# Performance work log

Measured on AMD Instinct MI355X. Metric: run time of the kernel, lower is better.

Reference implementation:

```python
import jax, jax.numpy as jnp
import numpy as np

B, CLN, QL, IH, IW = 64, 32, 32, 16, 16
CDF, SL = 256, 128
IDF = CLN * IH * IW  # 8192


def setup_inputs() -> dict:
    key = jax.random.key(0)
    k1, k2, k3 = jax.random.split(key, 3)
    inp = jax.random.normal(k1, (B, CLN, QL, IH, IW), dtype=jnp.float32)
    context = jax.random.normal(k2, (B, CDF, SL), dtype=jnp.float32)
    # Conv2d(cdf, idf, 1, bias=False) weight, squeezed to [idf, cdf]
    W = jax.random.normal(k3, (IDF, CDF), dtype=jnp.float32) * (1.0 / np.sqrt(CDF))
    return {"input": inp, "context": context, "W": W}


def reference(input, context, W):
    b, cln, queryL, ih, iw = input.shape
    idf = cln * ih * iw
    sourceL = context.shape[2]
    # target: b x queryL x (cln*ih*iw)
    targetT = jnp.transpose(input, (0, 2, 1, 3, 4)).reshape(b, queryL, idf)
    # 1x1 conv projection of context: b x idf x sourceL
    sourceT = jnp.einsum('oc,bcs->bos', W, context)
    # attention scores and softmax over sourceL (nn.Softmax on 2D -> dim=1)
    attn = jnp.einsum('bqd,bds->bqs', targetT, sourceT)  # b x queryL x sourceL
    attn = jax.nn.softmax(attn, axis=-1)
    attnT = jnp.transpose(attn, (0, 2, 1))  # b x sourceL x queryL
    # weighted context: b x idf x queryL
    wc = jnp.einsum('bds,bsq->bdq', sourceT, attnT)
    # faithful to torch .view: raw row-major reinterpretation of [b, idf, queryL]
    wc = wc.reshape(b, queryL, cln, ih, iw)
    wc = jnp.transpose(wc, (0, 2, 1, 3, 4))  # b x cln x queryL x ih x iw
    return (wc, attnT)
```

## Files before the change

kernel.cpp:

```cpp
#include <hip/hip_runtime.h>
#include <math.h>


#define ZK 16

typedef _Float16 f16x8 __attribute__((ext_vector_type(8)));
typedef __fp16 h16x2 __attribute__((ext_vector_type(2)));
typedef float f32x4 __attribute__((ext_vector_type(4)));

#define GLDS16(gp, lp)                                                          \
    __builtin_amdgcn_global_load_lds(                                           \
        (const __attribute__((address_space(1))) void*)(gp),                    \
        (__attribute__((address_space(3))) void*)(lp), 16, 0, 0)

__global__ __launch_bounds__(256) void k0a_prep(const float* __restrict__ Wm,
                                                _Float16* __restrict__ Wth,
                                                _Float16* __restrict__ Wtl) {
    const int kb = blockIdx.x;
    const int t = threadIdx.x;
    __shared__ float tile[32][260];
    {
        const int r = t >> 3;
        const int c0 = (t & 7) * 32;
        const float* src = Wm + (long)(kb * 32 + r) * 256 + c0;
#pragma unroll
        for (int i = 0; i < 8; ++i) {
            float4 v = *(const float4*)(src + i * 4);
            tile[r][c0 + i * 4 + 0] = v.x;
            tile[r][c0 + i * 4 + 1] = v.y;
            tile[r][c0 + i * 4 + 2] = v.z;
            tile[r][c0 + i * 4 + 3] = v.w;
        }
    }
    __syncthreads();
    const int lane = t & 63;
    const int quad = lane >> 4, l15 = lane & 15;
#pragma unroll
    for (int i = 0; i < 4; ++i) {
        int nsub = (t >> 6) * 4 + i;
        f16x8 oh, ol;
#pragma unroll
        for (int j = 0; j < 8; ++j) {
            float f = tile[quad * 8 + j][nsub * 16 + l15];
            _Float16 h = (_Float16)f;
            oh[j] = h;
            ol[j] = (_Float16)(f - (float)h);
        }
        long addr = ((long)(kb * 16 + nsub) * 64 + lane) * 8;
        *(f16x8*)(Wth + addr) = oh;
        *(f16x8*)(Wtl + addr) = ol;
    }
}

__global__ __launch_bounds__(256) void k0b_prep(const float* __restrict__ Wm,
                                                _Float16* __restrict__ Wbf) {
    const int t = threadIdx.x;
    const int fid = blockIdx.x * 4 + (t >> 6);
    const int mb = fid >> 3, kb4 = fid & 7;
    const int lane = t & 63;
    const int quad = lane >> 4, l15 = lane & 15;
    const float* src = Wm + (long)(mb * 16 + l15) * 256 + kb4 * 32 + quad * 8;
    float4 u0 = *(const float4*)(src);
    float4 u1 = *(const float4*)(src + 4);
    f16x8 o;
    o[0] = (_Float16)u0.x; o[1] = (_Float16)u0.y;
    o[2] = (_Float16)u0.z; o[3] = (_Float16)u0.w;
    o[4] = (_Float16)u1.x; o[5] = (_Float16)u1.y;
    o[6] = (_Float16)u1.z; o[7] = (_Float16)u1.w;
    *(f16x8*)(Wbf + ((long)fid * 64 + lane) * 8) = o;
}

__global__ __launch_bounds__(256, 2) void k1_mfma(const float* __restrict__ inp,
                                                  const _Float16* __restrict__ Wth,
                                                  const _Float16* __restrict__ Wtl,
                                                  float* __restrict__ tWpart) {
    const int kz = blockIdx.x;
    const int m0 = blockIdx.y * 64;
    const int t = threadIdx.x;
    const int lane = t & 63, wv = t >> 6;
    const int quad = lane >> 4, l15 = lane & 15;

    __shared__ _Float16 Fh[2][4][64][8];
    __shared__ _Float16 Fl[2][4][64][8];

    const float* arow;
    {
        const int mA = m0 + (t >> 2);
        arow = inp + (long)(mA >> 5) * 262144 + (long)(mA & 31) * 256 + (t & 3) * 8;
    }
    _Float16* wh = &Fh[0][t >> 6][((t & 3) << 4) | ((t >> 2) & 15)][0];
    _Float16* wl = &Fl[0][t >> 6][((t & 3) << 4) | ((t >> 2) & 15)][0];

    f32x4 acc[4][4];
#pragma unroll
    for (int i = 0; i < 4; ++i)
#pragma unroll
        for (int j = 0; j < 4; ++j) acc[i][j] = (f32x4){0.f, 0.f, 0.f, 0.f};

    float4 Ar[2][2];
    f16x8 Bh[2][4], Bl[2][4];

    {
        const int kg = kz * 512;
        const long off = (long)(kg >> 8) * 8192 + (kg & 255);
        Ar[0][0] = *(const float4*)(arow + off);
        Ar[0][1] = *(const float4*)(arow + off + 4);
        const long bb = ((long)((kz * 16) * 16 + wv * 4) * 64 + lane) * 8;
#pragma unroll
        for (int j = 0; j < 4; ++j) {
            Bh[0][j] = *(const f16x8*)(Wth + bb + (long)j * 512);
            Bl[0][j] = *(const f16x8*)(Wtl + bb + (long)j * 512);
        }
    }

#pragma unroll
    for (int it = 0; it < 16; ++it) {
        const int cur = it & 1, nxt = cur ^ 1;
        if (it < 15) {
            const int kg = kz * 512 + (it + 1) * 32;
            const long off = (long)(kg >> 8) * 8192 + (kg & 255);
            Ar[nxt][0] = *(const float4*)(arow + off);
            Ar[nxt][1] = *(const float4*)(arow + off + 4);
            const long bb = ((long)((kz * 16 + it + 1) * 16 + wv * 4) * 64 + lane) * 8;
#pragma unroll
            for (int j = 0; j < 4; ++j) {
                Bh[nxt][j] = *(const f16x8*)(Wth + bb + (long)j * 512);
                Bl[nxt][j] = *(const f16x8*)(Wtl + bb + (long)j * 512);
            }
        }
        __builtin_amdgcn_sched_barrier(0);

        {
            const float4 a0 = Ar[cur][0], a1 = Ar[cur][1];
            h16x2 h01 = __builtin_amdgcn_cvt_pkrtz(a0.x, a0.y);
            h16x2 h23 = __builtin_amdgcn_cvt_pkrtz(a0.z, a0.w);
            h16x2 h45 = __builtin_amdgcn_cvt_pkrtz(a1.x, a1.y);
            h16x2 h67 = __builtin_amdgcn_cvt_pkrtz(a1.z, a1.w);
            h16x2 l01 = __builtin_amdgcn_cvt_pkrtz(a0.x - (float)h01[0], a0.y - (float)h01[1]);
            h16x2 l23 = __builtin_amdgcn_cvt_pkrtz(a0.z - (float)h23[0], a0.w - (float)h23[1]);
            h16x2 l45 = __builtin_amdgcn_cvt_pkrtz(a1.x - (float)h45[0], a1.y - (float)h45[1]);
            h16x2 l67 = __builtin_amdgcn_cvt_pkrtz(a1.z - (float)h67[0], a1.w - (float)h67[1]);
            union { f16x8 v; h16x2 p[4]; } H, L;
            H.p[0] = h01; H.p[1] = h23; H.p[2] = h45; H.p[3] = h67;
            L.p[0] = l01; L.p[1] = l23; L.p[2] = l45; L.p[3] = l67;
            *(f16x8*)(wh + cur * 2048) = H.v;
            *(f16x8*)(wl + cur * 2048) = L.v;
        }
        asm volatile("s_waitcnt lgkmcnt(0)" ::: "memory");
        __builtin_amdgcn_sched_barrier(0);
        __builtin_amdgcn_s_barrier();
        __builtin_amdgcn_sched_barrier(0);

        f16x8 ah[4], al[4];
#pragma unroll
        for (int i = 0; i < 4; ++i) {
            ah[i] = *(const f16x8*)&Fh[cur][i][lane][0];
            al[i] = *(const f16x8*)&Fl[cur][i][lane][0];
        }
#pragma unroll
        for (int i = 0; i < 4; ++i)
#pragma unroll
            for (int j = 0; j < 4; ++j)
                acc[i][j] = __builtin_amdgcn_mfma_f32_16x16x32_f16(ah[i], Bh[cur][j], acc[i][j], 0, 0, 0);
#pragma unroll
        for (int i = 0; i < 4; ++i)
#pragma unroll
            for (int j = 0; j < 4; ++j)
                acc[i][j] = __builtin_amdgcn_mfma_f32_16x16x32_f16(al[i], Bh[cur][j], acc[i][j], 0, 0, 0);
#pragma unroll
        for (int i = 0; i < 4; ++i)
#pragma unroll
            for (int j = 0; j < 4; ++j)
                acc[i][j] = __builtin_amdgcn_mfma_f32_16x16x32_f16(ah[i], Bl[cur][j], acc[i][j], 0, 0, 0);
    }

    float* outp = tWpart + (long)kz * 524288;
#pragma unroll
    for (int i = 0; i < 4; ++i) {
        const int mbase = m0 + i * 16 + quad * 4;
#pragma unroll
        for (int j = 0; j < 4; ++j) {
            const int c = (wv * 4 + j) * 16 + l15;
#pragma unroll
            for (int rg = 0; rg < 4; ++rg)
                outp[(long)(mbase + rg) * 256 + c] = acc[i][j][rg];
        }
    }
}

__global__ __launch_bounds__(256) void k2_logits_softmax(const float* __restrict__ tWpart,
                                                         const float* __restrict__ ctx,
                                                         float* __restrict__ attnT) {
    const int b  = blockIdx.x;
    const int qg = blockIdx.y;
    const int t  = threadIdx.x;
    __shared__ float tw4[4][256];
    {
        const int q = t >> 6;
        const int c4 = (t & 63) * 4;
        const float* p = tWpart + (long)(b * 32 + qg * 4 + q) * 256 + c4;
        float4 s = make_float4(0.f, 0.f, 0.f, 0.f);
#pragma unroll
        for (int z = 0; z < ZK; ++z) {
            float4 v = *(const float4*)(p + (long)z * 524288);
            s.x += v.x; s.y += v.y; s.z += v.z; s.w += v.w;
        }
        *(float4*)&tw4[q][c4] = s;
    }
    __syncthreads();
    const int q = t >> 6, lane = t & 63;
    const float* ctxb = ctx + (long)b * 32768 + lane * 2;
    float ax0 = 0.f, ay0 = 0.f, ax1 = 0.f, ay1 = 0.f;
#pragma unroll 8
    for (int c = 0; c < 128; ++c) {
        float twa = tw4[q][c];
        float twb = tw4[q][c + 128];
        float2 cva = *(const float2*)(ctxb + c * 128);
        float2 cvb = *(const float2*)(ctxb + (c + 128) * 128);
        ax0 = fmaf(twa, cva.x, ax0);
        ay0 = fmaf(twa, cva.y, ay0);
        ax1 = fmaf(twb, cvb.x, ax1);
        ay1 = fmaf(twb, cvb.y, ay1);
    }
    float ax = ax0 + ax1, ay = ay0 + ay1;
    float mx = fmaxf(ax, ay);
#pragma unroll
    for (int m = 1; m <= 32; m <<= 1) mx = fmaxf(mx, __shfl_xor(mx, m));
    float ex = expf(ax - mx);
    float ey = expf(ay - mx);
    float sm = ex + ey;
#pragma unroll
    for (int m = 1; m <= 32; m <<= 1) sm += __shfl_xor(sm, m);
    float inv = 1.f / sm;
    ex *= inv; ey *= inv;
    float* o = attnT + (long)b * 4096 + (qg * 4 + q);
    o[(lane * 2 + 0) * 32] = ex;
    o[(lane * 2 + 1) * 32] = ey;
}

__global__ __launch_bounds__(256) void k3_ctxA(const float* __restrict__ ctx,
                                               const float* __restrict__ attnT,
                                               _Float16* __restrict__ ctxAqf) {
    const int cg = blockIdx.x;
    const int b  = blockIdx.y;
    const int t  = threadIdx.x;
    __shared__ float at[128][32];
    __shared__ float cs[32][132];
#pragma unroll
    for (int i = 0; i < 4; ++i)
        *(float4*)((float*)at + i * 1024 + t * 4) =
            *(const float4*)(attnT + (long)b * 4096 + i * 1024 + t * 4);
#pragma unroll
    for (int i = 0; i < 4; ++i) {
        int idx = i * 256 + t;
        int c = idx >> 5, sseg = (idx & 31) * 4;
        *(float4*)&cs[c][sseg] = *(const float4*)(ctx + (long)b * 32768 + (long)(cg * 32 + c) * 128 + sseg);
    }
    __syncthreads();
    const int c = t >> 3;
    const int qs = (t & 7) * 4;
    float4 acc = make_float4(0.f, 0.f, 0.f, 0.f);
#pragma unroll 4
    for (int s = 0; s < 128; ++s) {
        float cv = cs[c][s];
        float4 av = *(const float4*)&at[s][qs];
        acc.x = fmaf(cv, av.x, acc.x);
        acc.y = fmaf(cv, av.y, acc.y);
        acc.z = fmaf(cv, av.z, acc.z);
        acc.w = fmaf(cv, av.w, acc.w);
    }
    const int cglob = cg * 32 + c;
    const long cpart = (long)(cglob >> 5) * 64 + 16 * ((cglob >> 3) & 3);
    float vals[4] = {acc.x, acc.y, acc.z, acc.w};
#pragma unroll
    for (int u = 0; u < 4; ++u) {
        int n = b * 32 + qs + u;
        long addr = ((long)(n >> 4) * 8 * 64 + cpart + (n & 15)) * 8 + (cglob & 7);
        ctxAqf[addr] = (_Float16)vals[u];
    }
}

__global__ __launch_bounds__(256) void k4_mfma(const _Float16* __restrict__ Wbf,
                                               const _Float16* __restrict__ ctxAqf,
                                               float* __restrict__ out0) {
    const int t = threadIdx.x;
    const int lane = t & 63, wv = t >> 6;
    const int mb = blockIdx.x * 4 + wv;
    const int nb0 = blockIdx.y * 8;

    __shared__ _Float16 Bs[32768];

    {
        const _Float16* gsrc = ctxAqf + (long)nb0 * 4096;
#pragma unroll
        for (int i = 0; i < 16; ++i) {
            const int chunk = i * 256 + wv * 64;
            GLDS16(gsrc + (long)chunk * 8 + lane * 8, Bs + chunk * 8);
        }
    }
    __syncthreads();

    const _Float16* abase = Wbf + ((long)mb * 8 * 64 + lane) * 8;

    f32x4 acc[8];
#pragma unroll
    for (int j = 0; j < 8; ++j) acc[j] = (f32x4){0.f, 0.f, 0.f, 0.f};

#pragma unroll
    for (int kb = 0; kb < 8; ++kb) {
        f16x8 af = *(const f16x8*)(abase + (long)kb * 512);
#pragma unroll
        for (int j = 0; j < 8; ++j) {
            f16x8 bf = *(const f16x8*)(Bs + (j * 8 + kb) * 512 + lane * 8);
            acc[j] = __builtin_amdgcn_mfma_f32_16x16x32_f16(af, bf, acc[j], 0, 0, 0);
        }
    }
    const int quad = lane >> 4, col = lane & 15;
#pragma unroll
    for (int j = 0; j < 8; ++j) {
        const int n = (nb0 + j) * 16 + col;
        float* ob = out0 + (long)(n >> 5) * 262144 + (n & 31);
#pragma unroll
        for (int rg = 0; rg < 4; ++rg) {
            const int d = mb * 16 + quad * 4 + rg;
            ob[(long)((d >> 3) & 31) * 8192 + (long)(d >> 8) * 256 + (long)(d & 7) * 32] = acc[j][rg];
        }
    }
}

extern "C" void kernel_launch(void* const* d_in, const int* in_sizes, int n_in,
                              void* d_out, int out_size, void* d_ws, size_t ws_size,
                              hipStream_t stream) {
    const float* inp = (const float*)d_in[0];
    const float* ctx = (const float*)d_in[1];
    const float* Wm  = (const float*)d_in[2];
    float* out0 = (float*)d_out;
    float* out1 = out0 + 16777216;

    float* wsf = (float*)d_ws;
    float* tWpart = wsf;
    _Float16* Wbf    = (_Float16*)wsf;
    _Float16* ctxAqf = (_Float16*)(wsf + 1048576);
    _Float16* Wth = (_Float16*)(wsf + 8388608);
    _Float16* Wtl = Wth + 2097152;

    hipLaunchKernelGGL(k0a_prep, dim3(256), dim3(256), 0, stream, Wm, Wth, Wtl);
    hipLaunchKernelGGL(k1_mfma, dim3(16, 32), dim3(256), 0, stream, inp, Wth, Wtl, tWpart);
    hipLaunchKernelGGL(k2_logits_softmax, dim3(64, 8), dim3(256), 0, stream, tWpart, ctx, out1);
    hipLaunchKernelGGL(k0b_prep, dim3(1024), dim3(256), 0, stream, Wm, Wbf);
    hipLaunchKernelGGL(k3_ctxA, dim3(8, 64), dim3(256), 0, stream, ctx, out1, ctxAqf);
    hipLaunchKernelGGL(k4_mfma, dim3(128, 16), dim3(256), 0, stream, Wbf, ctxAqf, out0);
}
```

Measured before the change: 196.4 us.

## Fuse weight prep kernels, deepen k1 A-prefetch, pad split-K partial stride

Merges the two weight-conversion kernels into one launch, using separate workspace regions when the workspace is large enough. Restructures the k1 MFMA loop so global A loads run two iterations ahead. The fp16 hi/lo conversion and LDS write for the next tile now happen after the barrier, removing one barrier wait per iteration, and the MFMA block runs at raised wave priority. It also pads the split-K partial stride to spread channel/bank conflicts, at the cost of more registers and a workspace-size-dependent code path.

```diff
diff --git a/kernel.cpp b/kernel.cpp
--- a/kernel.cpp
+++ b/kernel.cpp
@@ -13,12 +13,10 @@
         (const __attribute__((address_space(1))) void*)(gp),                    \
         (__attribute__((address_space(3))) void*)(lp), 16, 0, 0)
 
-__global__ __launch_bounds__(256) void k0a_prep(const float* __restrict__ Wm,
-                                                _Float16* __restrict__ Wth,
-                                                _Float16* __restrict__ Wtl) {
-    const int kb = blockIdx.x;
-    const int t = threadIdx.x;
-    __shared__ float tile[32][260];
+__device__ __forceinline__ void k0a_body(const float* __restrict__ Wm,
+                                         _Float16* __restrict__ Wth,
+                                         _Float16* __restrict__ Wtl,
+                                         int kb, int t, float (*tile)[260]) {
     {
         const int r = t >> 3;
         const int c0 = (t & 7) * 32;
@@ -52,10 +50,10 @@
     }
 }
 
-__global__ __launch_bounds__(256) void k0b_prep(const float* __restrict__ Wm,
-                                                _Float16* __restrict__ Wbf) {
-    const int t = threadIdx.x;
-    const int fid = blockIdx.x * 4 + (t >> 6);
+__device__ __forceinline__ void k0b_body(const float* __restrict__ Wm,
+                                         _Float16* __restrict__ Wbf,
+                                         int bx, int t) {
+    const int fid = bx * 4 + (t >> 6);
     const int mb = fid >> 3, kb4 = fid & 7;
     const int lane = t & 63;
     const int quad = lane >> 4, l15 = lane & 15;
@@ -70,10 +68,30 @@
     *(f16x8*)(Wbf + ((long)fid * 64 + lane) * 8) = o;
 }
 
+__global__ __launch_bounds__(256) void k0a_prep(const float* __restrict__ Wm,
+                                                _Float16* __restrict__ Wth,
+                                                _Float16* __restrict__ Wtl) {
+    __shared__ float tile[32][260];
+    k0a_body(Wm, Wth, Wtl, blockIdx.x, threadIdx.x, tile);
+}
+__global__ __launch_bounds__(256) void k0b_prep(const float* __restrict__ Wm,
+                                                _Float16* __restrict__ Wbf) {
+    k0b_body(Wm, Wbf, blockIdx.x, threadIdx.x);
+}
+__global__ __launch_bounds__(256) void k0_all(const float* __restrict__ Wm,
+                                              _Float16* __restrict__ Wth,
+                                              _Float16* __restrict__ Wtl,
+                                              _Float16* __restrict__ Wbf) {
+    __shared__ float tile[32][260];
+    if (blockIdx.x < 256) k0a_body(Wm, Wth, Wtl, blockIdx.x, threadIdx.x, tile);
+    else                  k0b_body(Wm, Wbf, blockIdx.x - 256, threadIdx.x);
+}
+
 __global__ __launch_bounds__(256, 2) void k1_mfma(const float* __restrict__ inp,
                                                   const _Float16* __restrict__ Wth,
                                                   const _Float16* __restrict__ Wtl,
-                                                  float* __restrict__ tWpart) {
+                                                  float* __restrict__ tWpart,
+                                                  const long zstride) {
     const int kz = blockIdx.x;
     const int m0 = blockIdx.y * 64;
     const int t = threadIdx.x;
@@ -100,27 +118,54 @@
     float4 Ar[2][2];
     f16x8 Bh[2][4], Bl[2][4];
 
+#define AOFF(kg) ((long)((kg) >> 8) * 8192 + ((kg) & 255))
+#define CVTHL(a0, a1, H, L)                                                     \
+    {                                                                           \
+        h16x2 h01 = __builtin_amdgcn_cvt_pkrtz(a0.x, a0.y);                     \
+        h16x2 h23 = __builtin_amdgcn_cvt_pkrtz(a0.z, a0.w);                     \
+        h16x2 h45 = __builtin_amdgcn_cvt_pkrtz(a1.x, a1.y);                     \
+        h16x2 h67 = __builtin_amdgcn_cvt_pkrtz(a1.z, a1.w);                     \
+        h16x2 l01 = __builtin_amdgcn_cvt_pkrtz(a0.x - (float)h01[0], a0.y - (float)h01[1]); \
+        h16x2 l23 = __builtin_amdgcn_cvt_pkrtz(a0.z - (float)h23[0], a0.w - (float)h23[1]); \
+        h16x2 l45 = __builtin_amdgcn_cvt_pkrtz(a1.x - (float)h45[0], a1.y - (float)h45[1]); \
+        h16x2 l67 = __builtin_amdgcn_cvt_pkrtz(a1.z - (float)h67[0], a1.w - (float)h67[1]); \
+        union { f16x8 v; h16x2 p[4]; } U, V;                                    \
+        U.p[0] = h01; U.p[1] = h23; U.p[2] = h45; U.p[3] = h67;                 \
+        V.p[0] = l01; V.p[1] = l23; V.p[2] = l45; V.p[3] = l67;                 \
+        H = U.v; L = V.v;                                                       \
+    }
+
     {
-        const int kg = kz * 512;
-        const long off = (long)(kg >> 8) * 8192 + (kg & 255);
-        Ar[0][0] = *(const float4*)(arow + off);
-        Ar[0][1] = *(const float4*)(arow + off + 4);
+        const int kg0 = kz * 512;
+        Ar[0][0] = *(const float4*)(arow + AOFF(kg0));
+        Ar[0][1] = *(const float4*)(arow + AOFF(kg0) + 4);
+        const int kg1 = kg0 + 32;
+        Ar[1][0] = *(const float4*)(arow + AOFF(kg1));
+        Ar[1][1] = *(const float4*)(arow + AOFF(kg1) + 4);
         const long bb = ((long)((kz * 16) * 16 + wv * 4) * 64 + lane) * 8;
 #pragma unroll
         for (int j = 0; j < 4; ++j) {
             Bh[0][j] = *(const f16x8*)(Wth + bb + (long)j * 512);
             Bl[0][j] = *(const f16x8*)(Wtl + bb + (long)j * 512);
         }
+        f16x8 H0, L0;
+        const float4 a0 = Ar[0][0], a1 = Ar[0][1];
+        CVTHL(a0, a1, H0, L0);
+        *(f16x8*)(wh) = H0;
+        *(f16x8*)(wl) = L0;
+        asm volatile("s_waitcnt lgkmcnt(0)" ::: "memory");
+        __builtin_amdgcn_sched_barrier(0);
     }
 
 #pragma unroll
     for (int it = 0; it < 16; ++it) {
         const int cur = it & 1, nxt = cur ^ 1;
+        if (it < 14) {
+            const int kg = kz * 512 + (it + 2) * 32;
+            Ar[cur][0] = *(const float4*)(arow + AOFF(kg));
+            Ar[cur][1] = *(const float4*)(arow + AOFF(kg) + 4);
+        }
         if (it < 15) {
-            const int kg = kz * 512 + (it + 1) * 32;
-            const long off = (long)(kg >> 8) * 8192 + (kg & 255);
-            Ar[nxt][0] = *(const float4*)(arow + off);
-            Ar[nxt][1] = *(const float4*)(arow + off + 4);
             const long bb = ((long)((kz * 16 + it + 1) * 16 + wv * 4) * 64 + lane) * 8;
 #pragma unroll
             for (int j = 0; j < 4; ++j) {
@@ -129,34 +174,26 @@
             }
         }
         __builtin_amdgcn_sched_barrier(0);
-
-        {
-            const float4 a0 = Ar[cur][0], a1 = Ar[cur][1];
-            h16x2 h01 = __builtin_amdgcn_cvt_pkrtz(a0.x, a0.y);
-            h16x2 h23 = __builtin_amdgcn_cvt_pkrtz(a0.z, a0.w);
-            h16x2 h45 = __builtin_amdgcn_cvt_pkrtz(a1.x, a1.y);
-            h16x2 h67 = __builtin_amdgcn_cvt_pkrtz(a1.z, a1.w);
-            h16x2 l01 = __builtin_amdgcn_cvt_pkrtz(a0.x - (float)h01[0], a0.y - (float)h01[1]);
-            h16x2 l23 = __builtin_amdgcn_cvt_pkrtz(a0.z - (float)h23[0], a0.w - (float)h23[1]);
-            h16x2 l45 = __builtin_amdgcn_cvt_pkrtz(a1.x - (float)h45[0], a1.y - (float)h45[1]);
-            h16x2 l67 = __builtin_amdgcn_cvt_pkrtz(a1.z - (float)h67[0], a1.w - (float)h67[1]);
-            union { f16x8 v; h16x2 p[4]; } H, L;
-            H.p[0] = h01; H.p[1] = h23; H.p[2] = h45; H.p[3] = h67;
-            L.p[0] = l01; L.p[1] = l23; L.p[2] = l45; L.p[3] = l67;
-            *(f16x8*)(wh + cur * 2048) = H.v;
-            *(f16x8*)(wl + cur * 2048) = L.v;
-        }
-        asm volatile("s_waitcnt lgkmcnt(0)" ::: "memory");
+        f16x8 Hn, Ln;
+        if (it < 15) {
+            const float4 a0 = Ar[nxt][0], a1 = Ar[nxt][1];
+            CVTHL(a0, a1, Hn, Ln);
+        }
         __builtin_amdgcn_sched_barrier(0);
         __builtin_amdgcn_s_barrier();
-        __builtin_amdgcn_sched_barrier(0);
-
+        if (it < 15) {
+            *(f16x8*)(wh + nxt * 2048) = Hn;
+            *(f16x8*)(wl + nxt * 2048) = Ln;
+        }
         f16x8 ah[4], al[4];
 #pragma unroll
         for (int i = 0; i < 4; ++i) {
             ah[i] = *(const f16x8*)&Fh[cur][i][lane][0];
             al[i] = *(const f16x8*)&Fl[cur][i][lane][0];
         }
+        asm volatile("s_waitcnt lgkmcnt(0)" ::: "memory");
+        __builtin_amdgcn_sched_barrier(0);
+        __builtin_amdgcn_s_setprio(1);
 #pragma unroll
         for (int i = 0; i < 4; ++i)
 #pragma unroll
@@ -172,9 +209,10 @@
 #pragma unroll
             for (int j = 0; j < 4; ++j)
                 acc[i][j] = __builtin_amdgcn_mfma_f32_16x16x32_f16(ah[i], Bl[cur][j], acc[i][j], 0, 0, 0);
-    }
-
-    float* outp = tWpart + (long)kz * 524288;
+        __builtin_amdgcn_s_setprio(0);
+    }
+
+    float* outp = tWpart + (long)kz * zstride;
 #pragma unroll
     for (int i = 0; i < 4; ++i) {
         const int mbase = m0 + i * 16 + quad * 4;
@@ -190,7 +228,8 @@
 
 __global__ __launch_bounds__(256) void k2_logits_softmax(const float* __restrict__ tWpart,
                                                          const float* __restrict__ ctx,
-                                                         float* __restrict__ attnT) {
+                                                         float* __restrict__ attnT,
+                                                         const long zstride) {
     const int b  = blockIdx.x;
     const int qg = blockIdx.y;
     const int t  = threadIdx.x;
@@ -202,7 +241,7 @@
         float4 s = make_float4(0.f, 0.f, 0.f, 0.f);
 #pragma unroll
         for (int z = 0; z < ZK; ++z) {
-            float4 v = *(const float4*)(p + (long)z * 524288);
+            float4 v = *(const float4*)(p + (long)z * zstride);
             s.x += v.x; s.y += v.y; s.z += v.z; s.w += v.w;
         }
         *(float4*)&tw4[q][c4] = s;
@@ -337,17 +376,36 @@
     float* out0 = (float*)d_out;
     float* out1 = out0 + 16777216;
 
-    float* wsf = (float*)d_ws;
-    float* tWpart = wsf;
-    _Float16* Wbf    = (_Float16*)wsf;
-    _Float16* ctxAqf = (_Float16*)(wsf + 1048576);
-    _Float16* Wth = (_Float16*)(wsf + 8388608);
-    _Float16* Wtl = Wth + 2097152;
-
-    hipLaunchKernelGGL(k0a_prep, dim3(256), dim3(256), 0, stream, Wm, Wth, Wtl);
-    hipLaunchKernelGGL(k1_mfma, dim3(16, 32), dim3(256), 0, stream, inp, Wth, Wtl, tWpart);
-    hipLaunchKernelGGL(k2_logits_softmax, dim3(64, 8), dim3(256), 0, stream, tWpart, ctx, out1);
-    hipLaunchKernelGGL(k0b_prep, dim3(1024), dim3(256), 0, stream, Wm, Wbf);
-    hipLaunchKernelGGL(k3_ctxA, dim3(8, 64), dim3(256), 0, stream, ctx, out1, ctxAqf);
-    hipLaunchKernelGGL(k4_mfma, dim3(128, 16), dim3(256), 0, stream, Wbf, ctxAqf, out0);
-}
+    char* wsb = (char*)d_ws;
+    const size_t BIG_NEED = 47255552ull;
+
+    if (ws_size >= BIG_NEED) {
+        const long zs = 524288 + 1088;
+        float*    tWpart = (float*)wsb;
+        _Float16* Wth    = (_Float16*)(wsb + 33624064);
+        _Float16* Wtl    = (_Float16*)(wsb + 37818368);
+        _Float16* Wbf    = (_Float16*)(wsb + 42012672);
+        _Float16* ctxAqf = (_Float16*)(wsb + 46206976);
+
+        hipLaunchKernelGGL(k0_all, dim3(1280), dim3(256), 0, stream, Wm, Wth, Wtl, Wbf);
+        hipLaunchKernelGGL(k1_mfma, dim3(16, 32), dim3(256), 0, stream, inp, Wth, Wtl, tWpart, zs);
+        hipLaunchKernelGGL(k2_logits_softmax, dim3(64, 8), dim3(256), 0, stream, tWpart, ctx, out1, zs);
+        hipLaunchKernelGGL(k3_ctxA, dim3(8, 64), dim3(256), 0, stream, ctx, out1, ctxAqf);
+        hipLaunchKernelGGL(k4_mfma, dim3(128, 16), dim3(256), 0, stream, Wbf, ctxAqf, out0);
+    } else {
+        const long zs = 524288;
+        float* wsf = (float*)d_ws;
+        float*    tWpart = wsf;
+        _Float16* Wbf    = (_Float16*)wsf;
+        _Float16* ctxAqf = (_Float16*)(wsf + 1048576);
+        _Float16* Wth    = (_Float16*)(wsf + 8388608);
+        _Float16* Wtl    = Wth + 2097152;
+
+        hipLaunchKernelGGL(k0a_prep, dim3(256), dim3(256), 0, stream, Wm, Wth, Wtl);
+        hipLaunchKernelGGL(k1_mfma, dim3(16, 32), dim3(256), 0, stream, inp, Wth, Wtl, tWpart, zs);
+        hipLaunchKernelGGL(k2_logits_softmax, dim3(64, 8), dim3(256), 0, stream, tWpart, ctx, out1, zs);
+        hipLaunchKernelGGL(k0b_prep, dim3(1024), dim3(256), 0, stream, Wm, Wbf);
+        hipLaunchKernelGGL(k3_ctxA, dim3(8, 64), dim3(256), 0, stream, ctx, out1, ctxAqf);
+        hipLaunchKernelGGL(k4_mfma, dim3(128, 16), dim3(256), 0, stream, Wbf, ctxAqf, out0);
+    }
+}
```

Measured after the change: 196.0 us. About the same (-0.2%).
